# Performance work log

Hardware: AMD Instinct MI355X
Metric: run time of the kernel (lower is better)

## Reference

```python
import jax, jax.numpy as jnp
import numpy as np

N = 50000
E = 800000
IN_DIM = 256
HID = 256
OUT_DIM = 2


def setup_inputs() -> dict:
    key = jax.random.key(0)
    ks = jax.random.split(key, 10)
    x = jax.random.normal(ks[0], (N, IN_DIM), dtype=jnp.float32)
    edge_index = jax.random.randint(ks[1], (2, E), 0, N, dtype=jnp.int64)
    # Glorot-ish scaling so activations stay well-conditioned through 4 layers
    def w(k, fan_in, fan_out):
        return jax.random.normal(k, (fan_in, fan_out), dtype=jnp.float32) / jnp.sqrt(jnp.float32(fan_in))
    return {
        "x": x,
        "edge_index": edge_index,
        "W0": w(ks[2], IN_DIM, HID), "b0": jnp.zeros((HID,), jnp.float32),
        "W1": w(ks[3], HID, HID),    "b1": jnp.zeros((HID,), jnp.float32),
        "W2": w(ks[4], HID, HID),    "b2": jnp.zeros((HID,), jnp.float32),
        "W3": w(ks[5], HID, OUT_DIM), "b3": jnp.zeros((OUT_DIM,), jnp.float32),
    }


def _gcn_norm(edge_index, n, dtype):
    # PyG gcn_norm with self-loops: deg over destination, norm = d^-1/2[src]*d^-1/2[dst]
    loops = jnp.arange(n, dtype=edge_index.dtype)
    src = jnp.concatenate([edge_index[0], loops])
    dst = jnp.concatenate([edge_index[1], loops])
    deg = jax.ops.segment_sum(jnp.ones_like(dst, dtype=dtype), dst, num_segments=n)
    dis = deg ** -0.5  # deg >= 1 due to self-loops
    norm = dis[src] * dis[dst]
    return src, dst, norm


def reference(x, edge_index, W0, b0, W1, b1, W2, b2, W3, b3):
    n = x.shape[0]
    src, dst, norm = _gcn_norm(edge_index, n, x.dtype)

    def conv(h, W, b):
        h = h @ W                              # [N, F_out] dense GEMM
        msg = h[src] * norm[:, None]           # edge-gather + scale
        agg = jax.ops.segment_sum(msg, dst, num_segments=n)  # scatter-add
        return agg + b

    h = jax.nn.relu(conv(x, W0, b0))
    h = jax.nn.relu(conv(h, W1, b1))
    h = jax.nn.relu(conv(h, W2, b2))
    return conv(h, W3, b3)
```

## Files before the change

kernel.cpp:

```cpp
#include <hip/hip_runtime.h>

#define N_NODES 50000
#define N_EDGES 800000

static inline int cdiv(int a, int b) { return (a + b - 1) / b; }

typedef __attribute__((ext_vector_type(8))) short bf16x8;
typedef __attribute__((ext_vector_type(4))) float f32x4;
typedef __attribute__((ext_vector_type(2))) float f32x2;
typedef __attribute__((ext_vector_type(4))) unsigned int u32x4;

static __device__ __forceinline__ unsigned short f2bf(float f) {
    unsigned int u = __float_as_uint(f);
    unsigned int r = (u + 0x7FFF + ((u >> 16) & 1)) >> 16;
    return (unsigned short)r;
}
static __device__ __forceinline__ float bf2f(unsigned short h) {
    return __uint_as_float((unsigned int)h << 16);
}
static __device__ __forceinline__ float bf_lo(unsigned int u) { return __uint_as_float(u << 16); }
static __device__ __forceinline__ float bf_hi(unsigned int u) { return __uint_as_float(u & 0xFFFF0000u); }

static __device__ __forceinline__ int2 ldnt2(const int2* p) {
    unsigned long long u = __builtin_nontemporal_load((const unsigned long long*)p);
    int2 r;
    r.x = (int)(u & 0xFFFFFFFFull);
    r.y = (int)(u >> 32);
    return r;
}

static __device__ __forceinline__ void acc8p(f32x2* acc, uint4 v, float wgt) {
    f32x2 w2;
    w2.x = wgt;
    w2.y = wgt;
    f32x2 p;
    p.x = bf_lo(v.x); p.y = bf_hi(v.x); acc[0] += p * w2;
    p.x = bf_lo(v.y); p.y = bf_hi(v.y); acc[1] += p * w2;
    p.x = bf_lo(v.z); p.y = bf_hi(v.z); acc[2] += p * w2;
    p.x = bf_lo(v.w); p.y = bf_hi(v.w); acc[3] += p * w2;
}


#define CNT_B (((N_EDGES) + 1023) / 1024)

__global__ __launch_bounds__(256) void k_init(const int* __restrict__ edst, int* cnt, int e,
                                              const float* __restrict__ W0,
                                              const float* __restrict__ W1,
                                              const float* __restrict__ W2,
                                              const float* __restrict__ b0,
                                              const float* __restrict__ b1,
                                              const float* __restrict__ b2,
                                              const float* __restrict__ W3,
                                              unsigned short* __restrict__ Wth,
                                              unsigned short* __restrict__ Wtl,
                                              float* __restrict__ bpw,
                                              const float* __restrict__ X,
                                              unsigned short* __restrict__ Xh, long total4) {
    if (blockIdx.x < CNT_B) {
        int i = (blockIdx.x * 256 + threadIdx.x) * 4;
        if (i + 3 < e) {
            int4 v = *(const int4*)(edst + i);
            atomicAdd(&cnt[v.x], 1);
            atomicAdd(&cnt[v.y], 1);
            atomicAdd(&cnt[v.z], 1);
            atomicAdd(&cnt[v.w], 1);
        } else {
            for (int k = i; k < e; ++k) atomicAdd(&cnt[edst[k]], 1);
        }
    } else if (blockIdx.x < CNT_B + 48) {
        __shared__ float tile[64][65];
        int wb = blockIdx.x - CNT_B;
        int layer = wb / 16;
        int tid = wb % 16;
        int ti = tid >> 2, tj = tid & 3;
        const float* W = layer == 0 ? W0 : (layer == 1 ? W1 : W2);
        int r0 = ti * 64, n0 = tj * 64;
        int rr = threadIdx.x >> 4;
        int cc = (threadIdx.x & 15) * 4;
#pragma unroll
        for (int j = 0; j < 4; ++j) {
            float4 v = *(const float4*)(W + (size_t)(r0 + rr + j * 16) * 256 + n0 + cc);
            tile[rr + j * 16][cc + 0] = v.x;
            tile[rr + j * 16][cc + 1] = v.y;
            tile[rr + j * 16][cc + 2] = v.z;
            tile[rr + j * 16][cc + 3] = v.w;
        }
        __syncthreads();
        int pl = threadIdx.x & 63;
        int ng = threadIdx.x >> 6;
        int kl = (layer != 0) ? ((pl & 3) * 16 + (pl >> 2)) : pl;
#pragma unroll
        for (int i = 0; i < 16; ++i) {
            int nl = ng * 16 + i;
            float v = tile[kl][nl];
            unsigned short h = f2bf(v);
            size_t o = (size_t)layer * 65536 + (size_t)(n0 + nl) * 256 + r0 + pl;
            Wth[o] = h;
            Wtl[o] = f2bf(v - bf2f(h));
        }
    } else if (blockIdx.x == CNT_B + 48) {
        int p = threadIdx.x;
        int pl = p & 63;
        int c = (p & ~63) + (pl & 3) * 16 + (pl >> 2);
        bpw[p] = b0[c];
        bpw[256 + p] = b1[c];
        bpw[512 + p] = b2[c];
        bpw[768 + p * 2 + 0] = W3[(size_t)c * 2 + 0];
        bpw[768 + p * 2 + 1] = W3[(size_t)c * 2 + 1];
    } else {
        long i = (long)(blockIdx.x - (CNT_B + 49)) * 256 + threadIdx.x;
        if (i >= total4) return;
        float4 v = *(const float4*)(X + i * 4);
        ushort4 h;
        h.x = f2bf(v.x);
        h.y = f2bf(v.y);
        h.z = f2bf(v.z);
        h.w = f2bf(v.w);
        *(ushort4*)(Xh + i * 4) = h;
    }
}


__global__ __launch_bounds__(256) void k_scan1(const int* __restrict__ cnt,
                                               int* __restrict__ row_ptr,
                                               float* __restrict__ dis,
                                               int* __restrict__ blk, int n) {
    __shared__ int sums[256];
    int t = threadIdx.x;
    int base = blockIdx.x * 1024 + t * 4;
    int c0 = 0, c1 = 0, c2 = 0, c3 = 0;
    if (base + 3 < n) {
        int4 v = *(const int4*)(cnt + base);
        c0 = v.x + 1; c1 = v.y + 1; c2 = v.z + 1; c3 = v.w + 1;
    } else {
        if (base + 0 < n) c0 = cnt[base + 0] + 1;
        if (base + 1 < n) c1 = cnt[base + 1] + 1;
        if (base + 2 < n) c2 = cnt[base + 2] + 1;
        if (base + 3 < n) c3 = cnt[base + 3] + 1;
    }
    int s = c0 + c1 + c2 + c3;
    sums[t] = s;
    __syncthreads();
    int x = s;
    for (int off = 1; off < 256; off <<= 1) {
        int y = (t >= off) ? sums[t - off] : 0;
        __syncthreads();
        x += y;
        sums[t] = x;
        __syncthreads();
    }
    int excl = x - s;
    if (base + 0 < n) { row_ptr[base + 0] = excl;                dis[base + 0] = rsqrtf((float)c0); }
    if (base + 1 < n) { row_ptr[base + 1] = excl + c0;           dis[base + 1] = rsqrtf((float)c1); }
    if (base + 2 < n) { row_ptr[base + 2] = excl + c0 + c1;      dis[base + 2] = rsqrtf((float)c2); }
    if (base + 3 < n) { row_ptr[base + 3] = excl + c0 + c1 + c2; dis[base + 3] = rsqrtf((float)c3); }
    if (t == 255) blk[blockIdx.x] = x;
}

__global__ __launch_bounds__(256) void k_scan2(int* __restrict__ blk,
                                               int* __restrict__ row_ptr_n, int nb) {
    __shared__ int sums[256];
    int t = threadIdx.x;
    int s = (t < nb) ? blk[t] : 0;
    sums[t] = s;
    __syncthreads();
    int x = s;
    for (int off = 1; off < 256; off <<= 1) {
        int y = (t >= off) ? sums[t - off] : 0;
        __syncthreads();
        x += y;
        sums[t] = x;
        __syncthreads();
    }
    if (t < nb) blk[t] = x - s;
    if (t == 255) row_ptr_n[0] = x;
}

__global__ __launch_bounds__(256) void k_scan3(int* __restrict__ row_ptr,
                                               int* __restrict__ pos,
                                               const int* __restrict__ blk, int n) {
    int base = blockIdx.x * 1024 + threadIdx.x * 4;
    int off = blk[blockIdx.x];
#pragma unroll
    for (int i = 0; i < 4; ++i) {
        int idx = base + i;
        if (idx < n) {
            int v = row_ptr[idx] + off;
            row_ptr[idx] = v;
            pos[idx] = v;
        }
    }
}

__global__ void k_fill(const int* __restrict__ esrc, const int* __restrict__ edst,
                       int* pos, const float* __restrict__ dis,
                       int2* __restrict__ eg, int e, int n) {
    int i = blockIdx.x * 256 + threadIdx.x;
    if (i < e) {
        int s = esrc[i], d = edst[i];
        int p = atomicAdd(&pos[d], 1);
        unsigned long long u = (unsigned long long)(unsigned int)s |
                               ((unsigned long long)(unsigned int)__float_as_int(dis[s] * dis[d]) << 32);
        __builtin_nontemporal_store(u, (unsigned long long*)&eg[p]);
    } else if (i < e + n) {
        int v = i - e;
        int p = atomicAdd(&pos[v], 1);
        float dv = dis[v];
        unsigned long long u = (unsigned long long)(unsigned int)v |
                               ((unsigned long long)(unsigned int)__float_as_int(dv * dv) << 32);
        __builtin_nontemporal_store(u, (unsigned long long*)&eg[p]);
    }
}


#define GEMM_RB 196
#define GEMM_GRID (((GEMM_RB + 7) / 8) * 32)

__global__ __launch_bounds__(256) void k_gemm_mfma(const unsigned short* __restrict__ Ah,
                                                   const unsigned short* __restrict__ Wth,
                                                   const unsigned short* __restrict__ Wtl,
                                                   unsigned short* __restrict__ C, int M) {
    __shared__ unsigned short Wh[64][264];
    __shared__ unsigned short Wl[64][136];
    int xcd = blockIdx.x & 7;
    int s5 = blockIdx.x >> 3;
    int colblk = s5 & 3;
    int rowblk = (s5 >> 2) * 8 + xcd;
    if (rowblk >= GEMM_RB) return;
    int c0 = colblk * 64;
    int m0 = rowblk * 256;
    int t = threadIdx.x;
    int sr = t >> 2;

    {
        int hk0 = (t & 3) * 64;
        const unsigned short* gh = Wth + (size_t)(c0 + sr) * 256 + hk0;
        unsigned short* lh = &Wh[sr][hk0];
#pragma unroll
        for (int i = 0; i < 8; ++i)
            *(uint4*)(lh + i * 8) = *(const uint4*)(gh + i * 8);
        int lk0 = (t & 3) * 32;
        const unsigned short* gl = Wtl + (size_t)(c0 + sr) * 256 + lk0;
        unsigned short* ll = &Wl[sr][lk0];
#pragma unroll
        for (int i = 0; i < 4; ++i)
            *(uint4*)(ll + i * 8) = *(const uint4*)(gl + i * 8);
    }
    __syncthreads();

    int lane = t & 63, wave = t >> 6;
    int quad = lane >> 4, l16 = lane & 15;

    const unsigned short* aph[4];
#pragma unroll
    for (int mt = 0; mt < 4; ++mt) {
        int m = m0 + wave * 64 + mt * 16 + l16;
        if (m >= M) m = M - 1;
        aph[mt] = Ah + (size_t)m * 256 + quad * 8;
    }

    f32x4 acc[4][4];
#pragma unroll
    for (int i = 0; i < 4; ++i)
#pragma unroll
        for (int j = 0; j < 4; ++j) acc[i][j] = (f32x4){0.f, 0.f, 0.f, 0.f};

#pragma unroll 2
    for (int kc = 0; kc < 4; ++kc) {
        int ko = kc * 32;
        bf16x8 ahf[4];
#pragma unroll
        for (int mt = 0; mt < 4; ++mt) ahf[mt] = *(const bf16x8*)(aph[mt] + ko);
#pragma unroll
        for (int nt = 0; nt < 4; ++nt) {
            bf16x8 bh = *(const bf16x8*)&Wh[nt * 16 + l16][ko + quad * 8];
            bf16x8 bl = *(const bf16x8*)&Wl[nt * 16 + l16][ko + quad * 8];
#pragma unroll
            for (int mt = 0; mt < 4; ++mt) {
                acc[mt][nt] = __builtin_amdgcn_mfma_f32_16x16x32_bf16(ahf[mt], bh, acc[mt][nt], 0, 0, 0);
                acc[mt][nt] = __builtin_amdgcn_mfma_f32_16x16x32_bf16(ahf[mt], bl, acc[mt][nt], 0, 0, 0);
            }
        }
    }

    __syncthreads();
    {
        int lk0 = (t & 3) * 32;
        const unsigned short* gl = Wtl + (size_t)(c0 + sr) * 256 + 128 + lk0;
        unsigned short* ll = &Wl[sr][lk0];
#pragma unroll
        for (int i = 0; i < 4; ++i)
            *(uint4*)(ll + i * 8) = *(const uint4*)(gl + i * 8);
    }
    __syncthreads();

#pragma unroll 2
    for (int kc = 4; kc < 8; ++kc) {
        int ko = kc * 32;
        int kol = ko - 128;
        bf16x8 ahf[4];
#pragma unroll
        for (int mt = 0; mt < 4; ++mt) ahf[mt] = *(const bf16x8*)(aph[mt] + ko);
#pragma unroll
        for (int nt = 0; nt < 4; ++nt) {
            bf16x8 bh = *(const bf16x8*)&Wh[nt * 16 + l16][ko + quad * 8];
            bf16x8 bl = *(const bf16x8*)&Wl[nt * 16 + l16][kol + quad * 8];
#pragma unroll
            for (int mt = 0; mt < 4; ++mt) {
                acc[mt][nt] = __builtin_amdgcn_mfma_f32_16x16x32_bf16(ahf[mt], bh, acc[mt][nt], 0, 0, 0);
                acc[mt][nt] = __builtin_amdgcn_mfma_f32_16x16x32_bf16(ahf[mt], bl, acc[mt][nt], 0, 0, 0);
            }
        }
    }

#pragma unroll
    for (int mt = 0; mt < 4; ++mt) {
#pragma unroll
        for (int r = 0; r < 4; ++r) {
            int row = m0 + wave * 64 + mt * 16 + quad * 4 + r;
            if (row < M) {
                ushort4 sv;
                sv.x = f2bf(acc[mt][0][r]);
                sv.y = f2bf(acc[mt][1][r]);
                sv.z = f2bf(acc[mt][2][r]);
                sv.w = f2bf(acc[mt][3][r]);
                *(ushort4*)(C + (size_t)row * 256 + c0 + l16 * 4) = sv;
            }
        }
    }
}


template <int MODE>
__global__ __launch_bounds__(256, 8) void k_agg256(const unsigned short* __restrict__ t,
                                                   const int* __restrict__ row_ptr,
                                                   const int2* __restrict__ eg,
                                                   const float* __restrict__ bp,
                                                   unsigned short* __restrict__ outh,
                                                   const float* __restrict__ w3p,
                                                   float* __restrict__ t2, int n) {
    int lane = threadIdx.x & 63;
    int wave = threadIdx.x >> 6;
    int node = blockIdx.x * 4 + wave;
    if (node >= n) return;
    int half = lane >> 5;
    int fl = lane & 31;
    int beg = row_ptr[node], end = row_ptr[node + 1];
    f32x2 acc2[4];
#pragma unroll
    for (int i = 0; i < 4; ++i) { acc2[i].x = 0.f; acc2[i].y = 0.f; }
    const unsigned short* tp = t + fl * 8;

    int e = beg + half;
    for (; e + 10 < end; e += 12) {
        int2 a0 = ldnt2(eg + e), a1 = ldnt2(eg + e + 2), a2 = ldnt2(eg + e + 4);
        int2 a3 = ldnt2(eg + e + 6), a4 = ldnt2(eg + e + 8), a5 = ldnt2(eg + e + 10);
        uint4 v0 = *(const uint4*)(tp + (size_t)a0.x * 256);
        uint4 v1 = *(const uint4*)(tp + (size_t)a1.x * 256);
        uint4 v2 = *(const uint4*)(tp + (size_t)a2.x * 256);
        uint4 v3 = *(const uint4*)(tp + (size_t)a3.x * 256);
        uint4 v4 = *(const uint4*)(tp + (size_t)a4.x * 256);
        uint4 v5 = *(const uint4*)(tp + (size_t)a5.x * 256);
        acc8p(acc2, v0, __int_as_float(a0.y));
        acc8p(acc2, v1, __int_as_float(a1.y));
        acc8p(acc2, v2, __int_as_float(a2.y));
        acc8p(acc2, v3, __int_as_float(a3.y));
        acc8p(acc2, v4, __int_as_float(a4.y));
        acc8p(acc2, v5, __int_as_float(a5.y));
    }
    for (; e + 6 < end; e += 8) {
        int2 a0 = ldnt2(eg + e), a1 = ldnt2(eg + e + 2);
        int2 a2 = ldnt2(eg + e + 4), a3 = ldnt2(eg + e + 6);
        uint4 v0 = *(const uint4*)(tp + (size_t)a0.x * 256);
        uint4 v1 = *(const uint4*)(tp + (size_t)a1.x * 256);
        uint4 v2 = *(const uint4*)(tp + (size_t)a2.x * 256);
        uint4 v3 = *(const uint4*)(tp + (size_t)a3.x * 256);
        acc8p(acc2, v0, __int_as_float(a0.y));
        acc8p(acc2, v1, __int_as_float(a1.y));
        acc8p(acc2, v2, __int_as_float(a2.y));
        acc8p(acc2, v3, __int_as_float(a3.y));
    }
    for (; e + 2 < end; e += 4) {
        int2 a0 = ldnt2(eg + e), a1 = ldnt2(eg + e + 2);
        uint4 v0 = *(const uint4*)(tp + (size_t)a0.x * 256);
        uint4 v1 = *(const uint4*)(tp + (size_t)a1.x * 256);
        acc8p(acc2, v0, __int_as_float(a0.y));
        acc8p(acc2, v1, __int_as_float(a1.y));
    }
    if (e < end) {
        int2 a0 = ldnt2(eg + e);
        uint4 v0 = *(const uint4*)(tp + (size_t)a0.x * 256);
        acc8p(acc2, v0, __int_as_float(a0.y));
    }

    float va[8];
#pragma unroll
    for (int i = 0; i < 4; ++i) { va[2 * i] = acc2[i].x; va[2 * i + 1] = acc2[i].y; }
#pragma unroll
    for (int i = 0; i < 8; ++i) va[i] += __shfl_xor(va[i], 32);

    if (MODE == 0) {
        if (half == 0) {
            float4 bA = *(const float4*)(bp + fl * 8);
            float4 bB = *(const float4*)(bp + fl * 8 + 4);
            float r0 = fmaxf(va[0] + bA.x, 0.f), r1 = fmaxf(va[1] + bA.y, 0.f);
            float r2 = fmaxf(va[2] + bA.z, 0.f), r3 = fmaxf(va[3] + bA.w, 0.f);
            float r4 = fmaxf(va[4] + bB.x, 0.f), r5 = fmaxf(va[5] + bB.y, 0.f);
            float r6 = fmaxf(va[6] + bB.z, 0.f), r7 = fmaxf(va[7] + bB.w, 0.f);
            u32x4 w;
            w.x = (unsigned)f2bf(r0) | ((unsigned)f2bf(r1) << 16);
            w.y = (unsigned)f2bf(r2) | ((unsigned)f2bf(r3) << 16);
            w.z = (unsigned)f2bf(r4) | ((unsigned)f2bf(r5) << 16);
            w.w = (unsigned)f2bf(r6) | ((unsigned)f2bf(r7) << 16);
            __builtin_nontemporal_store(w, (u32x4*)(outh + (size_t)node * 256 + fl * 8));
        }
    } else {
        float4 bA = *(const float4*)(bp + fl * 8);
        float4 bB = *(const float4*)(bp + fl * 8 + 4);
        float r0 = fmaxf(va[0] + bA.x, 0.f), r1 = fmaxf(va[1] + bA.y, 0.f);
        float r2 = fmaxf(va[2] + bA.z, 0.f), r3 = fmaxf(va[3] + bA.w, 0.f);
        float r4 = fmaxf(va[4] + bB.x, 0.f), r5 = fmaxf(va[5] + bB.y, 0.f);
        float r6 = fmaxf(va[6] + bB.z, 0.f), r7 = fmaxf(va[7] + bB.w, 0.f);
        const float* wp = w3p + fl * 16;
        float4 wA = *(const float4*)(wp + 0);
        float4 wB = *(const float4*)(wp + 4);
        float4 wC = *(const float4*)(wp + 8);
        float4 wD = *(const float4*)(wp + 12);
        float s0 = r0 * wA.x + r1 * wA.z + r2 * wB.x + r3 * wB.z +
                   r4 * wC.x + r5 * wC.z + r6 * wD.x + r7 * wD.z;
        float s1 = r0 * wA.y + r1 * wA.w + r2 * wB.y + r3 * wB.w +
                   r4 * wC.y + r5 * wC.w + r6 * wD.y + r7 * wD.w;
#pragma unroll
        for (int off = 16; off > 0; off >>= 1) {
            s0 += __shfl_xor(s0, off);
            s1 += __shfl_xor(s1, off);
        }
        if (lane == 0) {
            f32x2 o;
            o.x = s0;
            o.y = s1;
            __builtin_nontemporal_store(o, (f32x2*)(t2 + (size_t)node * 2));
        }
    }
}


__global__ void k_agg2(const float* __restrict__ t2,
                       const int* __restrict__ row_ptr,
                       const int2* __restrict__ eg,
                       const float* __restrict__ b3,
                       float* __restrict__ out, int n) {
    int tid = blockIdx.x * 256 + threadIdx.x;
    int node = tid >> 2;
    int sub = tid & 3;
    if (node >= n) return;
    int beg = row_ptr[node], end = row_ptr[node + 1];
    float a0 = 0.f, a1 = 0.f;
    for (int e = beg + sub; e < end; e += 4) {
        int2 m = ldnt2(eg + e);
        float w = __int_as_float(m.y);
        float2 v = *(const float2*)(t2 + (size_t)m.x * 2);
        a0 += w * v.x;
        a1 += w * v.y;
    }
    a0 += __shfl_xor(a0, 1); a1 += __shfl_xor(a1, 1);
    a0 += __shfl_xor(a0, 2); a1 += __shfl_xor(a1, 2);
    if (sub == 0) {
        out[(size_t)node * 2 + 0] = a0 + b3[0];
        out[(size_t)node * 2 + 1] = a1 + b3[1];
    }
}


extern "C" void kernel_launch(void* const* d_in, const int* in_sizes, int n_in,
                              void* d_out, int out_size, void* d_ws, size_t ws_size,
                              hipStream_t stream) {
    const int N = N_NODES, E = N_EDGES;
    const float* x  = (const float*)d_in[0];
    const int* ei   = (const int*)d_in[1];
    const int* esrc = ei;
    const int* edst = ei + E;
    const float* W0 = (const float*)d_in[2];
    const float* b0 = (const float*)d_in[3];
    const float* W1 = (const float*)d_in[4];
    const float* b1 = (const float*)d_in[5];
    const float* W2 = (const float*)d_in[6];
    const float* b2 = (const float*)d_in[7];
    const float* W3 = (const float*)d_in[8];
    const float* b3 = (const float*)d_in[9];
    float* out = (float*)d_out;

    unsigned short* Ahh = (unsigned short*)d_ws;
    unsigned short* Tb  = Ahh + (size_t)N * 256;
    unsigned short* Wth = Tb + (size_t)N * 256;
    unsigned short* Wtl = Wth + 3 * 65536;
    int2*  eg     = (int2*)(Wtl + 3 * 65536);
    float* t2     = (float*)(eg + (E + N));
    float* bpw    = t2 + (size_t)N * 2;
    float* dis    = bpw + 1280;
    int*   cnt    = (int*)(dis + N);
    int*   row_ptr= cnt + N;
    int*   pos    = row_ptr + (N + 1);
    int*   blk    = pos + N;

    const int NB = cdiv(N, 1024);
    const long total4 = (long)N * 64;
    const int CA = cdiv((int)total4, 256);

    hipMemsetAsync(cnt, 0, (size_t)N * sizeof(int), stream);
    k_init<<<CNT_B + 49 + CA, 256, 0, stream>>>(edst, cnt, E,
                                                W0, W1, W2, b0, b1, b2, W3,
                                                Wth, Wtl, bpw, x, Ahh, total4);
    k_scan1<<<NB, 256, 0, stream>>>(cnt, row_ptr, dis, blk, N);
    k_scan2<<<1, 256, 0, stream>>>(blk, row_ptr + N, NB);
    k_scan3<<<NB, 256, 0, stream>>>(row_ptr, pos, blk, N);
    k_fill<<<cdiv(E + N, 256), 256, 0, stream>>>(esrc, edst, pos, dis, eg, E, N);

    const int agrid = cdiv(N, 4);

    k_gemm_mfma<<<GEMM_GRID, 256, 0, stream>>>(Ahh, Wth, Wtl, Tb, N);
    k_agg256<0><<<agrid, 256, 0, stream>>>(Tb, row_ptr, eg, bpw, Ahh, nullptr, nullptr, N);
    k_gemm_mfma<<<GEMM_GRID, 256, 0, stream>>>(Ahh, Wth + 65536, Wtl + 65536, Tb, N);
    k_agg256<0><<<agrid, 256, 0, stream>>>(Tb, row_ptr, eg, bpw + 256, Ahh, nullptr, nullptr, N);
    k_gemm_mfma<<<GEMM_GRID, 256, 0, stream>>>(Ahh, Wth + 2 * 65536, Wtl + 2 * 65536, Tb, N);
    k_agg256<1><<<agrid, 256, 0, stream>>>(Tb, row_ptr, eg, bpw + 512, nullptr, bpw + 768, t2, N);
    k_agg2<<<cdiv(4 * N, 256), 256, 0, stream>>>(t2, row_ptr, eg, b3, out, N);
}
```

Before: 460.8 us.

## Fuse x bf16 conversion into first GEMM and merge scans into decoupled lookback

The separate pass that converted x from fp32 to bf16 is removed. The first GEMM now reads fp32 x directly and converts to bf16 in registers. The three-kernel scan is also replaced by one kernel that chains block prefixes through flag and prefix arrays, removing two launches. In exchange, the first GEMM loads twice the A bytes, and the chained scan serialises blocks and assumes earlier blocks are resident to avoid deadlock (NB is only 49, so this is safe here).

```diff
diff --git a/kernel.cpp b/kernel.cpp
--- a/kernel.cpp
+++ b/kernel.cpp
@@ -53,9 +53,7 @@
                                               const float* __restrict__ W3,
                                               unsigned short* __restrict__ Wth,
                                               unsigned short* __restrict__ Wtl,
-                                              float* __restrict__ bpw,
-                                              const float* __restrict__ X,
-                                              unsigned short* __restrict__ Xh, long total4) {
+                                              float* __restrict__ bpw) {
     if (blockIdx.x < CNT_B) {
         int i = (blockIdx.x * 256 + threadIdx.x) * 4;
         if (i + 3 < e) {
@@ -98,7 +96,7 @@
             Wth[o] = h;
             Wtl[o] = f2bf(v - bf2f(h));
         }
-    } else if (blockIdx.x == CNT_B + 48) {
+    } else {
         int p = threadIdx.x;
         int pl = p & 63;
         int c = (p & ~63) + (pl & 3) * 16 + (pl >> 2);
@@ -107,27 +105,21 @@
         bpw[512 + p] = b2[c];
         bpw[768 + p * 2 + 0] = W3[(size_t)c * 2 + 0];
         bpw[768 + p * 2 + 1] = W3[(size_t)c * 2 + 1];
-    } else {
-        long i = (long)(blockIdx.x - (CNT_B + 49)) * 256 + threadIdx.x;
-        if (i >= total4) return;
-        float4 v = *(const float4*)(X + i * 4);
-        ushort4 h;
-        h.x = f2bf(v.x);
-        h.y = f2bf(v.y);
-        h.z = f2bf(v.z);
-        h.w = f2bf(v.w);
-        *(ushort4*)(Xh + i * 4) = h;
-    }
-}
-
-
-__global__ __launch_bounds__(256) void k_scan1(const int* __restrict__ cnt,
-                                               int* __restrict__ row_ptr,
-                                               float* __restrict__ dis,
-                                               int* __restrict__ blk, int n) {
+    }
+}
+
+
+__global__ __launch_bounds__(256) void k_scan(const int* __restrict__ cnt,
+                                              int* __restrict__ row_ptr,
+                                              float* __restrict__ dis,
+                                              int* __restrict__ pos,
+                                              int* __restrict__ pref,
+                                              int* __restrict__ flag, int n, int nb) {
     __shared__ int sums[256];
+    __shared__ int sprefix;
     int t = threadIdx.x;
-    int base = blockIdx.x * 1024 + t * 4;
+    int b = blockIdx.x;
+    int base = b * 1024 + t * 4;
     int c0 = 0, c1 = 0, c2 = 0, c3 = 0;
     if (base + 3 < n) {
         int4 v = *(const int4*)(cnt + base);
@@ -150,46 +142,26 @@
         __syncthreads();
     }
     int excl = x - s;
-    if (base + 0 < n) { row_ptr[base + 0] = excl;                dis[base + 0] = rsqrtf((float)c0); }
-    if (base + 1 < n) { row_ptr[base + 1] = excl + c0;           dis[base + 1] = rsqrtf((float)c1); }
-    if (base + 2 < n) { row_ptr[base + 2] = excl + c0 + c1;      dis[base + 2] = rsqrtf((float)c2); }
-    if (base + 3 < n) { row_ptr[base + 3] = excl + c0 + c1 + c2; dis[base + 3] = rsqrtf((float)c3); }
-    if (t == 255) blk[blockIdx.x] = x;
-}
-
-__global__ __launch_bounds__(256) void k_scan2(int* __restrict__ blk,
-                                               int* __restrict__ row_ptr_n, int nb) {
-    __shared__ int sums[256];
-    int t = threadIdx.x;
-    int s = (t < nb) ? blk[t] : 0;
-    sums[t] = s;
+    if (t == 255) {
+        int total = x;
+        int prefix = 0;
+        if (b > 0) {
+            while (atomicAdd(&flag[b - 1], 0) == 0) {}
+            prefix = atomicAdd(&pref[b - 1], 0);
+        }
+        atomicExch(&pref[b], prefix + total);
+        __threadfence();
+        atomicExch(&flag[b], 1);
+        sprefix = prefix;
+        if (b == nb - 1) row_ptr[n] = prefix + total;
+    }
     __syncthreads();
-    int x = s;
-    for (int off = 1; off < 256; off <<= 1) {
-        int y = (t >= off) ? sums[t - off] : 0;
-        __syncthreads();
-        x += y;
-        sums[t] = x;
-        __syncthreads();
-    }
-    if (t < nb) blk[t] = x - s;
-    if (t == 255) row_ptr_n[0] = x;
-}
-
-__global__ __launch_bounds__(256) void k_scan3(int* __restrict__ row_ptr,
-                                               int* __restrict__ pos,
-                                               const int* __restrict__ blk, int n) {
-    int base = blockIdx.x * 1024 + threadIdx.x * 4;
-    int off = blk[blockIdx.x];
-#pragma unroll
-    for (int i = 0; i < 4; ++i) {
-        int idx = base + i;
-        if (idx < n) {
-            int v = row_ptr[idx] + off;
-            row_ptr[idx] = v;
-            pos[idx] = v;
-        }
-    }
+    int prefix = sprefix;
+    int e0 = excl + prefix;
+    if (base + 0 < n) { row_ptr[base + 0] = e0;                pos[base + 0] = e0;                dis[base + 0] = rsqrtf((float)c0); }
+    if (base + 1 < n) { row_ptr[base + 1] = e0 + c0;           pos[base + 1] = e0 + c0;           dis[base + 1] = rsqrtf((float)c1); }
+    if (base + 2 < n) { row_ptr[base + 2] = e0 + c0 + c1;      pos[base + 2] = e0 + c0 + c1;      dis[base + 2] = rsqrtf((float)c2); }
+    if (base + 3 < n) { row_ptr[base + 3] = e0 + c0 + c1 + c2; pos[base + 3] = e0 + c0 + c1 + c2; dis[base + 3] = rsqrtf((float)c3); }
 }
 
 __global__ void k_fill(const int* __restrict__ esrc, const int* __restrict__ edst,
@@ -216,7 +188,8 @@
 #define GEMM_RB 196
 #define GEMM_GRID (((GEMM_RB + 7) / 8) * 32)
 
-__global__ __launch_bounds__(256) void k_gemm_mfma(const unsigned short* __restrict__ Ah,
+template <int AF32>
+__global__ __launch_bounds__(256) void k_gemm_mfma(const void* __restrict__ Ain,
                                                    const unsigned short* __restrict__ Wth,
                                                    const unsigned short* __restrict__ Wtl,
                                                    unsigned short* __restrict__ C, int M) {
@@ -252,11 +225,13 @@
     int quad = lane >> 4, l16 = lane & 15;
 
     const unsigned short* aph[4];
+    const float* apf[4];
 #pragma unroll
     for (int mt = 0; mt < 4; ++mt) {
         int m = m0 + wave * 64 + mt * 16 + l16;
         if (m >= M) m = M - 1;
-        aph[mt] = Ah + (size_t)m * 256 + quad * 8;
+        if (AF32) apf[mt] = (const float*)Ain + (size_t)m * 256 + quad * 8;
+        else      aph[mt] = (const unsigned short*)Ain + (size_t)m * 256 + quad * 8;
     }
 
     f32x4 acc[4][4];
@@ -270,7 +245,20 @@
         int ko = kc * 32;
         bf16x8 ahf[4];
 #pragma unroll
-        for (int mt = 0; mt < 4; ++mt) ahf[mt] = *(const bf16x8*)(aph[mt] + ko);
+        for (int mt = 0; mt < 4; ++mt) {
+            if (AF32) {
+                float4 f0 = *(const float4*)(apf[mt] + ko);
+                float4 f1 = *(const float4*)(apf[mt] + ko + 4);
+                bf16x8 v;
+                v[0] = (short)f2bf(f0.x); v[1] = (short)f2bf(f0.y);
+                v[2] = (short)f2bf(f0.z); v[3] = (short)f2bf(f0.w);
+                v[4] = (short)f2bf(f1.x); v[5] = (short)f2bf(f1.y);
+                v[6] = (short)f2bf(f1.z); v[7] = (short)f2bf(f1.w);
+                ahf[mt] = v;
+            } else {
+                ahf[mt] = *(const bf16x8*)(aph[mt] + ko);
+            }
+        }
 #pragma unroll
         for (int nt = 0; nt < 4; ++nt) {
             bf16x8 bh = *(const bf16x8*)&Wh[nt * 16 + l16][ko + quad * 8];
@@ -300,7 +288,20 @@
         int kol = ko - 128;
         bf16x8 ahf[4];
 #pragma unroll
-        for (int mt = 0; mt < 4; ++mt) ahf[mt] = *(const bf16x8*)(aph[mt] + ko);
+        for (int mt = 0; mt < 4; ++mt) {
+            if (AF32) {
+                float4 f0 = *(const float4*)(apf[mt] + ko);
+                float4 f1 = *(const float4*)(apf[mt] + ko + 4);
+                bf16x8 v;
+                v[0] = (short)f2bf(f0.x); v[1] = (short)f2bf(f0.y);
+                v[2] = (short)f2bf(f0.z); v[3] = (short)f2bf(f0.w);
+                v[4] = (short)f2bf(f1.x); v[5] = (short)f2bf(f1.y);
+                v[6] = (short)f2bf(f1.z); v[7] = (short)f2bf(f1.w);
+                ahf[mt] = v;
+            } else {
+                ahf[mt] = *(const bf16x8*)(aph[mt] + ko);
+            }
+        }
 #pragma unroll
         for (int nt = 0; nt < 4; ++nt) {
             bf16x8 bh = *(const bf16x8*)&Wh[nt * 16 + l16][ko + quad * 8];
@@ -499,30 +500,27 @@
     float* bpw    = t2 + (size_t)N * 2;
     float* dis    = bpw + 1280;
     int*   cnt    = (int*)(dis + N);
-    int*   row_ptr= cnt + N;
+    int*   flag   = cnt + N;
+    int*   pref   = flag + 64;
+    int*   row_ptr= pref + 64;
     int*   pos    = row_ptr + (N + 1);
-    int*   blk    = pos + N;
 
     const int NB = cdiv(N, 1024);
-    const long total4 = (long)N * 64;
-    const int CA = cdiv((int)total4, 256);
-
-    hipMemsetAsync(cnt, 0, (size_t)N * sizeof(int), stream);
-    k_init<<<CNT_B + 49 + CA, 256, 0, stream>>>(edst, cnt, E,
-                                                W0, W1, W2, b0, b1, b2, W3,
-                                                Wth, Wtl, bpw, x, Ahh, total4);
-    k_scan1<<<NB, 256, 0, stream>>>(cnt, row_ptr, dis, blk, N);
-    k_scan2<<<1, 256, 0, stream>>>(blk, row_ptr + N, NB);
-    k_scan3<<<NB, 256, 0, stream>>>(row_ptr, pos, blk, N);
+
+    hipMemsetAsync(cnt, 0, (size_t)(N + 64) * sizeof(int), stream);
+    k_init<<<CNT_B + 49, 256, 0, stream>>>(edst, cnt, E,
+                                           W0, W1, W2, b0, b1, b2, W3,
+                                           Wth, Wtl, bpw);
+    k_scan<<<NB, 256, 0, stream>>>(cnt, row_ptr, dis, pos, pref, flag, N, NB);
     k_fill<<<cdiv(E + N, 256), 256, 0, stream>>>(esrc, edst, pos, dis, eg, E, N);
 
     const int agrid = cdiv(N, 4);
 
-    k_gemm_mfma<<<GEMM_GRID, 256, 0, stream>>>(Ahh, Wth, Wtl, Tb, N);
+    k_gemm_mfma<1><<<GEMM_GRID, 256, 0, stream>>>(x, Wth, Wtl, Tb, N);
     k_agg256<0><<<agrid, 256, 0, stream>>>(Tb, row_ptr, eg, bpw, Ahh, nullptr, nullptr, N);
-    k_gemm_mfma<<<GEMM_GRID, 256, 0, stream>>>(Ahh, Wth + 65536, Wtl + 65536, Tb, N);
+    k_gemm_mfma<0><<<GEMM_GRID, 256, 0, stream>>>(Ahh, Wth + 65536, Wtl + 65536, Tb, N);
     k_agg256<0><<<agrid, 256, 0, stream>>>(Tb, row_ptr, eg, bpw + 256, Ahh, nullptr, nullptr, N);
-    k_gemm_mfma<<<GEMM_GRID, 256, 0, stream>>>(Ahh, Wth + 2 * 65536, Wtl + 2 * 65536, Tb, N);
+    k_gemm_mfma<0><<<GEMM_GRID, 256, 0, stream>>>(Ahh, Wth + 2 * 65536, Wtl + 2 * 65536, Tb, N);
     k_agg256<1><<<agrid, 256, 0, stream>>>(Tb, row_ptr, eg, bpw + 512, nullptr, bpw + 768, t2, N);
     k_agg2<<<cdiv(4 * N, 256), 256, 0, stream>>>(t2, row_ptr, eg, b3, out, N);
 }
```

Measured after the change: 517.6 us. 1.12x slower.
